# Kernel optimization log

Measured on AMD Instinct MI355X. Metric: run time of the kernel, lower is better.

The kernel has to match this reference:

```python
import jax, jax.numpy as jnp
import numpy as np

N_NODES = 50000
N_EDGES = 1600000
HIDDEN = 256
N_GRAPHS = 1024
N_PROPS = 8
N_FEAT = 4
IN_DIM = N_FEAT + 4 * 8 + 4 * 8  # 68


def setup_inputs() -> dict:
    key = jax.random.key(0)
    ks = jax.random.split(key, 20)
    s = 0.05
    inp = {
        "x": jax.random.randint(ks[0], (N_NODES, N_FEAT), 0, 720),
        "edge_index": jax.random.randint(ks[1], (2, N_EDGES), 0, N_NODES),
        "batch": jnp.sort(jax.random.randint(ks[2], (N_NODES,), 0, N_GRAPHS)),
        "emb24": jax.random.normal(ks[3], (24, 8), jnp.float32) * s,
        "emb72": jax.random.normal(ks[4], (72, 8), jnp.float32) * s,
        "lin1_w": jax.random.normal(ks[5], (HIDDEN, IN_DIM), jnp.float32) * s,
        "lin1_b": jnp.zeros((HIDDEN,), jnp.float32),
        "qa1_w": jax.random.normal(ks[6], (HIDDEN, HIDDEN), jnp.float32) * s,
        "qa1_b": jnp.zeros((HIDDEN,), jnp.float32),
        "lin2_w": jax.random.normal(ks[7], (HIDDEN, HIDDEN), jnp.float32) * s,
        "lin2_b": jnp.zeros((HIDDEN,), jnp.float32),
        "qa2_w": jax.random.normal(ks[8], (HIDDEN, HIDDEN), jnp.float32) * s,
        "qa2_b": jnp.zeros((HIDDEN,), jnp.float32),
        "head_w1": jax.random.normal(ks[9], (N_PROPS, HIDDEN // 2, HIDDEN), jnp.float32) * s,
        "head_b1": jnp.zeros((N_PROPS, HIDDEN // 2), jnp.float32),
        "head_w2": jax.random.normal(ks[10], (N_PROPS, 1, HIDDEN // 2), jnp.float32) * s,
        "head_b2": jnp.zeros((N_PROPS, 1), jnp.float32),
    }
    return inp


def _qagcn_conv(h, src, dst, lin_w, lin_b, qa_w, qa_b):
    n = h.shape[0]
    lin_x = h @ lin_w.T + lin_b                                  # [N, H]
    # message = lin(x_j); aggr='add' over edges; add_self_loops contributes
    # one extra lin_x per node, and update() adds lin(x) again -> 2*lin_x.
    aggr = jax.ops.segment_sum(lin_x[src], dst, num_segments=n)  # [N, H]
    h2 = aggr + 2.0 * lin_x
    b, e, _, _ = jnp.split(h2, 4, axis=-1)
    h3 = jnp.concatenate([b, e, b + e, b + 2.0 * e], axis=-1)
    return jax.nn.relu(h3 @ qa_w.T + qa_b)


def reference(x, edge_index, batch, emb24, emb72, lin1_w, lin1_b, qa1_w, qa1_b,
              lin2_w, lin2_b, qa2_w, qa2_b, head_w1, head_b1, head_w2, head_b2):
    n = x.shape[0]
    r24 = emb24[x % 24].reshape(n, -1)          # [N, 32]
    r72 = emb72[x % 72].reshape(n, -1)          # [N, 32]
    h = jnp.concatenate([x.astype(jnp.float32), r24, r72], axis=-1)  # [N, 68]
    src, dst = edge_index[0], edge_index[1]
    h = _qagcn_conv(h, src, dst, lin1_w, lin1_b, qa1_w, qa1_b)
    h = _qagcn_conv(h, src, dst, lin2_w, lin2_b, qa2_w, qa2_b)
    # global mean pool over graphs
    sums = jax.ops.segment_sum(h, batch, num_segments=N_GRAPHS)      # [G, H]
    cnts = jax.ops.segment_sum(jnp.ones((n,), h.dtype), batch, num_segments=N_GRAPHS)
    g = sums / jnp.maximum(cnts, 1.0)[:, None]                       # [G, H]
    # per-property 2-layer MLP heads
    h1 = jax.nn.relu(jnp.einsum('gd,phd->pgh', g, head_w1) + head_b1[:, None, :])
    out = jnp.einsum('pgh,poh->pgo', h1, head_w2) + head_b2[:, None, :]  # [P, G, 1]
    return out[..., 0].T                                             # [G, P]
```

## Files before the change

kernel.cpp:

```cpp
#include <hip/hip_runtime.h>
#include <hip/hip_bf16.h>

#define N_NODESC 50000
#define N_EDGESC 1600000
#define NGC 1024
#define NPC 8
#define NBIN 196
#define NBLKE 391

typedef __attribute__((ext_vector_type(8))) short bf16x8;
typedef __attribute__((ext_vector_type(4))) float f32x4;

__device__ inline ushort f2bf(float f) {
  union { float f; uint u; } v; v.f = f;
  uint u = v.u;
  u += 0x7FFF + ((u >> 16) & 1);
  return (ushort)(u >> 16);
}
__device__ inline float bflo(uint u) {
  union { uint u; float f; } v; v.u = u << 16; return v.f;
}
__device__ inline float bfhi(uint u) {
  union { uint u; float f; } v; v.u = u & 0xFFFF0000u; return v.f;
}

__global__ __launch_bounds__(256) void megaprep(
    const float* __restrict__ qa1w, const float* __restrict__ qa2w,
    const float* __restrict__ lin1w, const float* __restrict__ lin2w,
    ushort* __restrict__ qe1, ushort* __restrict__ qe2,
    ushort* __restrict__ l1w, ushort* __restrict__ l2w,
    const int* __restrict__ x, const float* __restrict__ e24,
    const float* __restrict__ e72, ushort* __restrict__ feat,
    const int* __restrict__ dst, int* __restrict__ bh) {
  int bid = blockIdx.x, t = threadIdx.x;
  if (bid < 256) {
    const float* qw = (bid < 128) ? qa1w : qa2w;
    ushort* eff = (bid < 128) ? qe1 : qe2;
    int k = (bid & 127) * 2 + (t >> 7);
    int j = t & 127;
    const float* r = qw + (size_t)k * 256;
    float v;
    if (j < 64) v = r[j] + r[128 + j] + r[192 + j];
    else { int j2 = j - 64; v = r[64 + j2] + r[128 + j2] + 2.0f * r[192 + j2]; }
    eff[(size_t)k * 128 + j] = f2bf(v);
  } else if (bid < 304) {
    int i = (bid - 256) * 256 + t;
    int r = i / 96, c = i - r * 96;
    l1w[i] = (c < 68) ? f2bf(lin1w[(size_t)r * 68 + c]) : (ushort)0;
  } else if (bid < 432) {
    int r = bid - 304;
    l2w[(size_t)r * 256 + t] = f2bf(lin2w[(size_t)r * 256 + t]);
  } else if (bid < 1456) {
    const int stride = 1024 * 256;
    for (int i = (bid - 432) * 256 + t; i < N_NODESC * 96; i += stride) {
      int n = i / 96, tt = i - n * 96;
      float v = 0.f;
      if (tt < 4) v = (float)x[n * 4 + tt];
      else if (tt < 36) { int kk = tt - 4;  int f = kk >> 3, c = kk & 7; v = e24[(x[n * 4 + f] % 24) * 8 + c]; }
      else if (tt < 68) { int kk = tt - 36; int f = kk >> 3, c = kk & 7; v = e72[(x[n * 4 + f] % 72) * 8 + c]; }
      feat[i] = f2bf(v);
    }
  } else {
    __shared__ int hist[NBIN];
    int blk = bid - 1456;
    if (t < NBIN) hist[t] = 0;
    __syncthreads();
    int base = blk * 4096;
#pragma unroll
    for (int i = 0; i < 16; ++i) {
      int idx = base + i * 256 + t;
      if (idx < N_EDGESC) atomicAdd(&hist[dst[idx] >> 8], 1);
    }
    __syncthreads();
    if (t < NBIN) bh[(size_t)t * NBLKE + blk] = hist[t];
  }
}

__global__ __launch_bounds__(64) void csr_scan_bins(int* __restrict__ bh, int* __restrict__ bt) {
  int bin = blockIdx.x;
  int lane = threadIdx.x;
  int carry = 0;
  int* row = bh + (size_t)bin * NBLKE;
  for (int c = 0; c < NBLKE; c += 64) {
    int j = c + lane;
    int v = (j < NBLKE) ? row[j] : 0;
    int incl = v;
#pragma unroll
    for (int off = 1; off < 64; off <<= 1) {
      int u = __shfl_up(incl, off, 64);
      if (lane >= off) incl += u;
    }
    if (j < NBLKE) row[j] = carry + incl - v;
    carry += __shfl(incl, 63, 64);
  }
  if (lane == 0) bt[bin] = carry;
}

template <int K>
__device__ __forceinline__ void gemm_body(ushort* ws, int bx, int by,
    const ushort* __restrict__ A, const ushort* __restrict__ W,
    const float* __restrict__ bias, ushort* __restrict__ C,
    int M, int NC, int relu) {
  int tid = threadIdx.x;
  int lane = tid & 63;
  int wv = tid >> 6;
  int rbase = bx * 128 + wv * 32;
  int colt = by * 128;
  int r16 = lane & 15;
  int kg = (lane >> 4) * 8;

  const char* wt = (const char*)(W + (size_t)colt * K);
#pragma unroll
  for (int i = 0; i < K / 16; ++i) {
    int o = (i * 256 + tid) * 16;
    int col = o / (2 * K);
    int sw = o ^ ((col & 7) << 4);
    *(bf16x8*)((char*)ws + sw) = *(const bf16x8*)(wt + o);
  }
  __syncthreads();

  f32x4 acc[2][8];
#pragma unroll
  for (int m = 0; m < 2; ++m)
#pragma unroll
    for (int n = 0; n < 8; ++n) acc[m][n] = (f32x4){0.f, 0.f, 0.f, 0.f};

  for (int k0 = 0; k0 < K; k0 += 32) {
    int ks = k0 + kg;
    bf16x8 a[2], b[8];
#pragma unroll
    for (int m = 0; m < 2; ++m) {
      int rr = rbase + m * 16 + r16;
      if (rr >= M) rr = M - 1;
      a[m] = *(const bf16x8*)(A + (size_t)rr * K + ks);
    }
#pragma unroll
    for (int n = 0; n < 8; ++n) {
      int cl = n * 16 + r16;
      int byte = (cl * 2 * K + ks * 2) ^ ((cl & 7) << 4);
      b[n] = *(const bf16x8*)((const char*)ws + byte);
    }
#pragma unroll
    for (int m = 0; m < 2; ++m)
#pragma unroll
      for (int n = 0; n < 8; ++n)
        acc[m][n] = __builtin_amdgcn_mfma_f32_16x16x32_bf16(a[m], b[n], acc[m][n], 0, 0, 0);
  }

  int rowoff = (lane >> 4) * 4;
#pragma unroll
  for (int m = 0; m < 2; ++m) {
#pragma unroll
    for (int j = 0; j < 4; ++j) {
      int row = rbase + m * 16 + rowoff + j;
      if (row >= M) continue;
#pragma unroll
      for (int n = 0; n < 8; ++n) {
        int col = colt + n * 16 + r16;
        float v = acc[m][n][j] + bias[col];
        if (relu) v = fmaxf(v, 0.f);
        C[(size_t)row * NC + col] = f2bf(v);
      }
    }
  }
}

template <int K>
__global__ __launch_bounds__(256, 2) void mfma_gemm_lds(
    const ushort* __restrict__ A, const ushort* __restrict__ W,
    const float* __restrict__ bias, ushort* __restrict__ C,
    int M, int NC, int relu) {
  __shared__ ushort ws[128 * K];
  gemm_body<K>(ws, blockIdx.x, blockIdx.y, A, W, bias, C, M, NC, relu);
}

__global__ __launch_bounds__(256, 2) void scatter_lin1(
    const int* __restrict__ src, const int* __restrict__ dst,
    const int* __restrict__ bh, const int* __restrict__ bt, uint* __restrict__ tmp,
    const ushort* __restrict__ feat, const ushort* __restrict__ l1w,
    const float* __restrict__ lin1b, ushort* __restrict__ linx) {
  __shared__ ushort ws[128 * 96];
  int bid = blockIdx.x, t = threadIdx.x;
  if (bid < NBLKE) {
    int* sc = (int*)ws;
    int* cur = sc + 256;
    int v = (t < NBIN) ? bt[t] : 0;
    sc[t] = v;
    __syncthreads();
    for (int off = 1; off < 256; off <<= 1) {
      int u = (t >= off) ? sc[t - off] : 0;
      __syncthreads();
      sc[t] += u;
      __syncthreads();
    }
    if (t < NBIN) cur[t] = (sc[t] - v) + bh[(size_t)t * NBLKE + bid];
    __syncthreads();
    int base = bid * 4096;
#pragma unroll
    for (int i = 0; i < 16; ++i) {
      int idx = base + i * 256 + t;
      if (idx < N_EDGESC) {
        int d = dst[idx];
        uint p = ((uint)d << 16) | (uint)src[idx];
        int pos = atomicAdd(&cur[d >> 8], 1);
        tmp[pos] = p;
      }
    }
  } else {
    gemm_body<96>(ws, bid - NBLKE, 0, feat, l1w, lin1b, linx, N_NODESC, 128, 0);
  }
}

__global__ __launch_bounds__(256) void csr_bucket_sort(const uint* __restrict__ tmp,
                                                       const int* __restrict__ bt,
                                                       ushort* __restrict__ elist,
                                                       int* __restrict__ rp) {
  __shared__ int sc[256];
  __shared__ int cnt[256];
  int b = blockIdx.x, t = threadIdx.x;
  int v = (t < NBIN) ? bt[t] : 0;
  sc[t] = v;
  __syncthreads();
  for (int off = 1; off < 256; off <<= 1) {
    int u = (t >= off) ? sc[t - off] : 0;
    __syncthreads();
    sc[t] += u;
    __syncthreads();
  }
  int base = (b == 0) ? 0 : sc[b - 1];
  int end = sc[b];
  int total = sc[NBIN - 1];
  __syncthreads();
  cnt[t] = 0;
  __syncthreads();
  for (int i = base + t; i < end; i += 256)
    atomicAdd(&cnt[(tmp[i] >> 16) & 255], 1);
  __syncthreads();
  int cv = cnt[t];
  sc[t] = cv;
  __syncthreads();
  for (int off = 1; off < 256; off <<= 1) {
    int u = (t >= off) ? sc[t - off] : 0;
    __syncthreads();
    sc[t] += u;
    __syncthreads();
  }
  int excl = sc[t] - cv;
  int node = (b << 8) + t;
  if (node < N_NODESC) rp[node] = base + excl;
  if (b == NBIN - 1 && t == 0) rp[N_NODESC] = total;
  cnt[t] = base + excl;
  __syncthreads();
  for (int i = base + t; i < end; i += 256) {
    uint p = tmp[i];
    int pos = atomicAdd(&cnt[(p >> 16) & 255], 1);
    elist[pos] = (ushort)(p & 0xFFFFu);
  }
}

__global__ __launch_bounds__(256, 4) void aggregate2(const uint* __restrict__ lx,
                                                     const int* __restrict__ rp,
                                                     const ushort* __restrict__ elist,
                                                     uint* __restrict__ h2) {
  int wv = threadIdx.x >> 6, lane = threadIdx.x & 63;
  int n = blockIdx.x * 4 + wv;
  int beg = rp[n], end = rp[n + 1];
  uint su = lx[(size_t)n * 64 + lane];
  float a0 = 2.f * bflo(su), a1 = 2.f * bfhi(su);
  int e = beg;
  for (; e + 32 <= end; e += 32) {
    uint r[32];
#pragma unroll
    for (int i = 0; i < 32; ++i) r[i] = lx[(size_t)elist[e + i] * 64 + lane];
    __builtin_amdgcn_sched_barrier(0);
#pragma unroll
    for (int i = 0; i < 32; ++i) { a0 += bflo(r[i]); a1 += bfhi(r[i]); }
  }
  for (; e + 8 <= end; e += 8) {
    uint r[8];
#pragma unroll
    for (int i = 0; i < 8; ++i) r[i] = lx[(size_t)elist[e + i] * 64 + lane];
    __builtin_amdgcn_sched_barrier(0);
#pragma unroll
    for (int i = 0; i < 8; ++i) { a0 += bflo(r[i]); a1 += bfhi(r[i]); }
  }
  for (; e < end; ++e) {
    uint r0 = lx[(size_t)elist[e] * 64 + lane];
    a0 += bflo(r0);
    a1 += bfhi(r0);
  }
  uint w = (uint)f2bf(a0) | ((uint)f2bf(a1) << 16);
  __builtin_nontemporal_store(w, h2 + (size_t)n * 64 + lane);
}

__global__ __launch_bounds__(256) void pool2(const uint* __restrict__ h,
                                             const int* __restrict__ batch,
                                             float* __restrict__ g) {
  int gg = blockIdx.x;
  int t = threadIdx.x;
  int j = t & 127, rg = t >> 7;
  int lo = 0, hi = N_NODESC;
  while (lo < hi) { int mid = (lo + hi) >> 1; if (batch[mid] < gg) lo = mid + 1; else hi = mid; }
  int beg = lo;
  hi = N_NODESC;
  while (lo < hi) { int mid = (lo + hi) >> 1; if (batch[mid] < gg + 1) lo = mid + 1; else hi = mid; }
  int end = lo;
  float a0 = 0.f, a1 = 0.f;
  int n = beg + rg;
  for (; n + 2 < end; n += 4) {
    uint u = h[(size_t)n * 128 + j];
    uint u2 = h[(size_t)(n + 2) * 128 + j];
    a0 += bflo(u) + bflo(u2);
    a1 += bfhi(u) + bfhi(u2);
  }
  if (n < end) {
    uint u = h[(size_t)n * 128 + j];
    a0 += bflo(u);
    a1 += bfhi(u);
  }
  __shared__ float s0[128], s1[128];
  if (rg == 1) { s0[j] = a0; s1[j] = a1; }
  __syncthreads();
  if (rg == 0) {
    a0 += s0[j];
    a1 += s1[j];
    float cfac = fmaxf((float)(end - beg), 1.0f);
    g[(size_t)gg * 256 + 2 * j] = a0 / cfac;
    g[(size_t)gg * 256 + 2 * j + 1] = a1 / cfac;
  }
}

__global__ __launch_bounds__(128) void head_kernel(const float* __restrict__ g,
    const float* __restrict__ w1, const float* __restrict__ b1,
    const float* __restrict__ w2, const float* __restrict__ b2,
    float* __restrict__ out) {
  int p = blockIdx.y;
  int g0 = blockIdx.x * 8;
  int t = threadIdx.x;
  __shared__ float gs[8][256];
  for (int i = t; i < 8 * 256; i += 128)
    gs[i >> 8][i & 255] = g[(size_t)(g0 + (i >> 8)) * 256 + (i & 255)];
  __syncthreads();
  const float4* w4 = (const float4*)(w1 + ((size_t)p * 128 + t) * 256);
  float bv = b1[p * 128 + t];
  float acc[8];
#pragma unroll
  for (int q = 0; q < 8; ++q) acc[q] = bv;
  for (int d4 = 0; d4 < 64; ++d4) {
    float4 wv = w4[d4];
#pragma unroll
    for (int q = 0; q < 8; ++q) {
      acc[q] += gs[q][d4 * 4 + 0] * wv.x + gs[q][d4 * 4 + 1] * wv.y +
                gs[q][d4 * 4 + 2] * wv.z + gs[q][d4 * 4 + 3] * wv.w;
    }
  }
  float w2v = w2[p * 128 + t];
  __shared__ float red[2][8];
  int wave = t >> 6, lane = t & 63;
#pragma unroll
  for (int q = 0; q < 8; ++q) {
    float v = fmaxf(acc[q], 0.f) * w2v;
    for (int o = 32; o > 0; o >>= 1) v += __shfl_down(v, o, 64);
    if (lane == 0) red[wave][q] = v;
  }
  __syncthreads();
  if (t < 8) out[(size_t)(g0 + t) * 8 + p] = red[0][t] + red[1][t] + b2[p];
}

extern "C" void kernel_launch(void* const* d_in, const int* in_sizes, int n_in,
                              void* d_out, int out_size, void* d_ws, size_t ws_size,
                              hipStream_t stream) {
  const int*   x     = (const int*)d_in[0];
  const int*   ei    = (const int*)d_in[1];
  const int*   batch = (const int*)d_in[2];
  const float* emb24 = (const float*)d_in[3];
  const float* emb72 = (const float*)d_in[4];
  const float* lin1w = (const float*)d_in[5];
  const float* lin1b = (const float*)d_in[6];
  const float* qa1w  = (const float*)d_in[7];
  const float* qa1b  = (const float*)d_in[8];
  const float* lin2w = (const float*)d_in[9];
  const float* lin2b = (const float*)d_in[10];
  const float* qa2w  = (const float*)d_in[11];
  const float* qa2b  = (const float*)d_in[12];
  const float* hw1   = (const float*)d_in[13];
  const float* hb1   = (const float*)d_in[14];
  const float* hw2   = (const float*)d_in[15];
  const float* hb2   = (const float*)d_in[16];
  float* out = (float*)d_out;

  const int* srcv = ei;
  const int* dstv = ei + N_EDGESC;

  char* wsb = (char*)d_ws;
  size_t off = 0;
  auto alloc = [&](size_t b) { char* p = wsb + off; off += (b + 255) & ~(size_t)255; return p; };
  ushort* feat  = (ushort*)alloc((size_t)N_NODESC * 96 * 2);
  ushort* linx  = (ushort*)alloc((size_t)N_NODESC * 128 * 2);
  ushort* h2    = (ushort*)alloc((size_t)N_NODESC * 128 * 2);
  ushort* h     = (ushort*)alloc((size_t)N_NODESC * 256 * 2);
  float*  gbuf  = (float*)alloc((size_t)NGC * 256 * 4);
  ushort* qe1   = (ushort*)alloc(256 * 128 * 2);
  ushort* qe2   = (ushort*)alloc(256 * 128 * 2);
  ushort* l1w   = (ushort*)alloc(128 * 96 * 2);
  ushort* l2w   = (ushort*)alloc(128 * 256 * 2);
  int*    rp    = (int*)alloc((size_t)(N_NODESC + 1) * 4);
  ushort* elist = (ushort*)alloc((size_t)N_EDGESC * 2);
  int*    bh    = (int*)alloc((size_t)NBIN * NBLKE * 4);
  int*    bt    = (int*)alloc((size_t)NBIN * 4);
  uint*   tmp   = (uint*)h;

  megaprep<<<1847, 256, 0, stream>>>(qa1w, qa2w, lin1w, lin2w, qe1, qe2, l1w, l2w,
                                     x, emb24, emb72, feat, dstv, bh);
  csr_scan_bins<<<NBIN, 64, 0, stream>>>(bh, bt);

  int gm = (N_NODESC + 127) / 128;

  scatter_lin1<<<NBLKE + gm, 256, 0, stream>>>(srcv, dstv, bh, bt, tmp,
                                               feat, l1w, lin1b, linx);
  csr_bucket_sort<<<NBIN, 256, 0, stream>>>(tmp, bt, elist, rp);

  aggregate2<<<N_NODESC / 4, 256, 0, stream>>>((const uint*)linx, rp, elist, (uint*)h2);
  mfma_gemm_lds<128><<<dim3(gm, 2), 256, 0, stream>>>(h2, qe1, qa1b, h, N_NODESC, 256, 1);

  mfma_gemm_lds<256><<<dim3(gm, 1), 256, 0, stream>>>(h, l2w, lin2b, linx, N_NODESC, 128, 0);
  aggregate2<<<N_NODESC / 4, 256, 0, stream>>>((const uint*)linx, rp, elist, (uint*)h2);
  mfma_gemm_lds<128><<<dim3(gm, 2), 256, 0, stream>>>(h2, qe2, qa2b, h, N_NODESC, 256, 1);

  pool2<<<NGC, 256, 0, stream>>>((const uint*)h, batch, gbuf);
  head_kernel<<<dim3(NGC / 8, NPC), 128, 0, stream>>>(gbuf, hw1, hb1, hw2, hb2, out);
}
```

Measured before the change: 254.4 us.

## Aggregate neighbor rows with 16-byte loads and split edges across quarter-waves

The CSR aggregation kernel now has each wavefront split into four 16-lane groups. Each group processes a different edge and loads a full 256-byte bf16 row using uint4 (16-byte) loads, and the partial sums are combined with cross-lane shuffles. The tail is handled by padding: a zeroed dummy row is appended to linx so out-of-range edges read zeros without branching. This aims for wider memory transactions and more gathers in flight per wave, at the cost of shuffle reductions, more registers, and idle lanes on the final store.

```diff
diff --git a/kernel.cpp b/kernel.cpp
--- a/kernel.cpp
+++ b/kernel.cpp
@@ -258,39 +258,62 @@
   }
 }
 
-__global__ __launch_bounds__(256, 4) void aggregate2(const uint* __restrict__ lx,
-                                                     const int* __restrict__ rp,
-                                                     const ushort* __restrict__ elist,
-                                                     uint* __restrict__ h2) {
+__global__ __launch_bounds__(256) void aggregate4(const uint4* __restrict__ LX,
+                                                  const int* __restrict__ rp,
+                                                  const ushort* __restrict__ elist,
+                                                  uint4* __restrict__ h2) {
   int wv = threadIdx.x >> 6, lane = threadIdx.x & 63;
+  int g = lane >> 4, l = lane & 15;
   int n = blockIdx.x * 4 + wv;
   int beg = rp[n], end = rp[n + 1];
-  uint su = lx[(size_t)n * 64 + lane];
-  float a0 = 2.f * bflo(su), a1 = 2.f * bfhi(su);
+  float a0 = 0.f, a1 = 0.f, a2 = 0.f, a3 = 0.f;
+  float a4 = 0.f, a5 = 0.f, a6 = 0.f, a7 = 0.f;
   int e = beg;
   for (; e + 32 <= end; e += 32) {
-    uint r[32];
-#pragma unroll
-    for (int i = 0; i < 32; ++i) r[i] = lx[(size_t)elist[e + i] * 64 + lane];
-    __builtin_amdgcn_sched_barrier(0);
-#pragma unroll
-    for (int i = 0; i < 32; ++i) { a0 += bflo(r[i]); a1 += bfhi(r[i]); }
-  }
-  for (; e + 8 <= end; e += 8) {
-    uint r[8];
-#pragma unroll
-    for (int i = 0; i < 8; ++i) r[i] = lx[(size_t)elist[e + i] * 64 + lane];
-    __builtin_amdgcn_sched_barrier(0);
-#pragma unroll
-    for (int i = 0; i < 8; ++i) { a0 += bflo(r[i]); a1 += bfhi(r[i]); }
-  }
-  for (; e < end; ++e) {
-    uint r0 = lx[(size_t)elist[e] * 64 + lane];
-    a0 += bflo(r0);
-    a1 += bfhi(r0);
-  }
-  uint w = (uint)f2bf(a0) | ((uint)f2bf(a1) << 16);
-  __builtin_nontemporal_store(w, h2 + (size_t)n * 64 + lane);
+    uint4 r[8];
+#pragma unroll
+    for (int i = 0; i < 8; ++i) {
+      int s = elist[e + i * 4 + g];
+      r[i] = LX[(size_t)s * 16 + l];
+    }
+#pragma unroll
+    for (int i = 0; i < 8; ++i) {
+      a0 += bflo(r[i].x); a1 += bfhi(r[i].x);
+      a2 += bflo(r[i].y); a3 += bfhi(r[i].y);
+      a4 += bflo(r[i].z); a5 += bfhi(r[i].z);
+      a6 += bflo(r[i].w); a7 += bfhi(r[i].w);
+    }
+  }
+  for (; e < end; e += 4) {
+    int idx = e + g;
+    int s = (idx < end) ? (int)elist[idx] : N_NODESC;
+    uint4 r = LX[(size_t)s * 16 + l];
+    a0 += bflo(r.x); a1 += bfhi(r.x);
+    a2 += bflo(r.y); a3 += bfhi(r.y);
+    a4 += bflo(r.z); a5 += bfhi(r.z);
+    a6 += bflo(r.w); a7 += bfhi(r.w);
+  }
+  a0 += __shfl_xor(a0, 16); a0 += __shfl_xor(a0, 32);
+  a1 += __shfl_xor(a1, 16); a1 += __shfl_xor(a1, 32);
+  a2 += __shfl_xor(a2, 16); a2 += __shfl_xor(a2, 32);
+  a3 += __shfl_xor(a3, 16); a3 += __shfl_xor(a3, 32);
+  a4 += __shfl_xor(a4, 16); a4 += __shfl_xor(a4, 32);
+  a5 += __shfl_xor(a5, 16); a5 += __shfl_xor(a5, 32);
+  a6 += __shfl_xor(a6, 16); a6 += __shfl_xor(a6, 32);
+  a7 += __shfl_xor(a7, 16); a7 += __shfl_xor(a7, 32);
+  if (g == 0) {
+    uint4 sv = LX[(size_t)n * 16 + l];
+    a0 += 2.f * bflo(sv.x); a1 += 2.f * bfhi(sv.x);
+    a2 += 2.f * bflo(sv.y); a3 += 2.f * bfhi(sv.y);
+    a4 += 2.f * bflo(sv.z); a5 += 2.f * bfhi(sv.z);
+    a6 += 2.f * bflo(sv.w); a7 += 2.f * bfhi(sv.w);
+    uint4 w;
+    w.x = (uint)f2bf(a0) | ((uint)f2bf(a1) << 16);
+    w.y = (uint)f2bf(a2) | ((uint)f2bf(a3) << 16);
+    w.z = (uint)f2bf(a4) | ((uint)f2bf(a5) << 16);
+    w.w = (uint)f2bf(a6) | ((uint)f2bf(a7) << 16);
+    h2[(size_t)n * 16 + l] = w;
+  }
 }
 
 __global__ __launch_bounds__(256) void pool2(const uint* __restrict__ h,
@@ -396,7 +419,7 @@
   size_t off = 0;
   auto alloc = [&](size_t b) { char* p = wsb + off; off += (b + 255) & ~(size_t)255; return p; };
   ushort* feat  = (ushort*)alloc((size_t)N_NODESC * 96 * 2);
-  ushort* linx  = (ushort*)alloc((size_t)N_NODESC * 128 * 2);
+  ushort* linx  = (ushort*)alloc((size_t)(N_NODESC + 1) * 128 * 2);
   ushort* h2    = (ushort*)alloc((size_t)N_NODESC * 128 * 2);
   ushort* h     = (ushort*)alloc((size_t)N_NODESC * 256 * 2);
   float*  gbuf  = (float*)alloc((size_t)NGC * 256 * 4);
@@ -410,6 +433,8 @@
   int*    bt    = (int*)alloc((size_t)NBIN * 4);
   uint*   tmp   = (uint*)h;
 
+  hipMemsetAsync(linx + (size_t)N_NODESC * 128, 0, 256, stream);
+
   megaprep<<<1847, 256, 0, stream>>>(qa1w, qa2w, lin1w, lin2w, qe1, qe2, l1w, l2w,
                                      x, emb24, emb72, feat, dstv, bh);
   csr_scan_bins<<<NBIN, 64, 0, stream>>>(bh, bt);
@@ -420,11 +445,11 @@
                                                feat, l1w, lin1b, linx);
   csr_bucket_sort<<<NBIN, 256, 0, stream>>>(tmp, bt, elist, rp);
 
-  aggregate2<<<N_NODESC / 4, 256, 0, stream>>>((const uint*)linx, rp, elist, (uint*)h2);
+  aggregate4<<<N_NODESC / 4, 256, 0, stream>>>((const uint4*)linx, rp, elist, (uint4*)h2);
   mfma_gemm_lds<128><<<dim3(gm, 2), 256, 0, stream>>>(h2, qe1, qa1b, h, N_NODESC, 256, 1);
 
   mfma_gemm_lds<256><<<dim3(gm, 1), 256, 0, stream>>>(h, l2w, lin2b, linx, N_NODESC, 128, 0);
-  aggregate2<<<N_NODESC / 4, 256, 0, stream>>>((const uint*)linx, rp, elist, (uint*)h2);
+  aggregate4<<<N_NODESC / 4, 256, 0, stream>>>((const uint4*)linx, rp, elist, (uint4*)h2);
   mfma_gemm_lds<128><<<dim3(gm, 2), 256, 0, stream>>>(h2, qe2, qa2b, h, N_NODESC, 256, 1);
 
   pool2<<<NGC, 256, 0, stream>>>((const uint*)h, batch, gbuf);
```

New measurement: 253.3 us. No clear change (-0.4%).
